# Kernel optimization log

Hardware: AMD Instinct MI355X
Metric: run time of the kernel (lower is better)

Reference implementation:

```python
import jax, jax.numpy as jnp
import numpy as np
from math import sqrt

V, D, H, HD, L, F, P, NL = 32000, 768, 12, 64, 12, 3072, 2048, 2
B, S = 8, 1024
EPS = 1e-5


def setup_inputs() -> dict:
    key = jax.random.key(0)
    ks = jax.random.split(key, 12)
    n = lambda k, sh: (jax.random.normal(k, sh, jnp.float32) * 0.02)
    return {
        'tokens': jax.random.randint(ks[0], (B, S), 0, V, dtype=jnp.int32),
        'tok_emb': n(ks[1], (V, D)),
        'pos_emb': n(ks[2], (P, D)),
        'emb_ln_s': jnp.ones((D,), jnp.float32), 'emb_ln_b': jnp.zeros((D,), jnp.float32),
        'Wq': n(ks[3], (L, H, D, HD)), 'bq': jnp.zeros((L, H, HD), jnp.float32),
        'Wk': n(ks[4], (L, H, D, HD)), 'bk': jnp.zeros((L, H, HD), jnp.float32),
        'Wv': n(ks[5], (L, H, D, HD)), 'bv': jnp.zeros((L, H, HD), jnp.float32),
        'Wo': n(ks[6], (L, D, D)), 'bo': jnp.zeros((L, D), jnp.float32),
        'ln1_s': jnp.ones((L, D), jnp.float32), 'ln1_b': jnp.zeros((L, D), jnp.float32),
        'ln2_s': jnp.ones((L, D), jnp.float32), 'ln2_b': jnp.zeros((L, D), jnp.float32),
        'W1': n(ks[7], (L, D, F)), 'b1': jnp.zeros((L, F), jnp.float32),
        'W2': n(ks[8], (L, F, D)), 'b2': jnp.zeros((L, D), jnp.float32),
        'Wc': n(ks[9], (D, NL)), 'bc': jnp.zeros((NL,), jnp.float32),
    }


def _ln(x, s, b):
    m = jnp.mean(x, -1, keepdims=True)
    v = jnp.mean((x - m) ** 2, -1, keepdims=True)
    return (x - m) * jax.lax.rsqrt(v + EPS) * s + b


def reference(tokens, tok_emb, pos_emb, emb_ln_s, emb_ln_b,
              Wq, bq, Wk, bk, Wv, bv, Wo, bo,
              ln1_s, ln1_b, ln2_s, ln2_b, W1, b1, W2, b2, Wc, bc):
    b, s = tokens.shape
    # embeddings (dropout is eval-mode identity)
    x = tok_emb[tokens] + pos_emb[:s][None, :, :]          # [b, s, D]
    x = _ln(x, emb_ln_s, emb_ln_b)
    scale = 1.0 / sqrt(HD)
    for l in range(L):
        xn = _ln(x, ln1_s[l], ln1_b[l])
        q = jnp.einsum('bsd,hdk->bhsk', xn, Wq[l]) + bq[l][:, None, :]
        k = jnp.einsum('bsd,hdk->bhsk', xn, Wk[l]) + bk[l][:, None, :]
        v = jnp.einsum('bsd,hdk->bhsk', xn, Wv[l]) + bv[l][:, None, :]
        scores = jnp.einsum('bhsk,bhtk->bhst', q, k) * scale   # [b,H,s,s]
        w = jax.nn.softmax(scores, axis=-1)
        o = jnp.einsum('bhst,bhtk->bhsk', w, v)                # [b,H,s,HD]
        o = o.transpose(0, 2, 1, 3).reshape(b, s, D)           # concat heads
        x = x + o @ Wo[l] + bo[l]
        xn = _ln(x, ln2_s[l], ln2_b[l])
        h = jax.nn.gelu(xn @ W1[l] + b1[l], approximate=False)
        x = x + h @ W2[l] + b2[l]
    # CLS token -> classifier (dropout identity)
    return x[:, 0, :] @ Wc + bc                                # [b, NL]
```

## Files before the change

### kernel.cpp

```cpp
#include <hip/hip_runtime.h>
#include <hip/hip_bf16.h>
#include <math.h>

#define B_   8
#define S_   1024
#define D_   768
#define H_   12
#define HD_  64
#define L_   12
#define F_   3072
#define NTOK 8192

typedef __bf16 bf16x8 __attribute__((ext_vector_type(8)));
typedef float  f32x4  __attribute__((ext_vector_type(4)));
typedef unsigned short u16;

static __device__ __forceinline__ unsigned short f2bf_bits(float f) {
    __hip_bfloat16 h = __float2bfloat16(f);
    return __builtin_bit_cast(unsigned short, h);
}
static __device__ __forceinline__ float bf2f(unsigned short u) {
    unsigned int t = ((unsigned int)u) << 16;
    return __builtin_bit_cast(float, t);
}
static __device__ __forceinline__ void gload16(const void* g, void* l) {
    __builtin_amdgcn_global_load_lds(
        (__attribute__((address_space(1))) void*)g,
        (__attribute__((address_space(3))) void*)l, 16, 0, 0);
}

__global__ __launch_bounds__(256)
void prep_ln_kernel(const float* __restrict__ Wq, const float* __restrict__ Wk,
                    const float* __restrict__ Wv, const float* __restrict__ Wo,
                    const float* __restrict__ W1, const float* __restrict__ W2,
                    int l, __hip_bfloat16* __restrict__ wbuf,
                    const float* __restrict__ xin, const float* __restrict__ gam,
                    const float* __restrict__ bet, __hip_bfloat16* __restrict__ xnout)
{
    __shared__ u16 T[64][68];
    if (blockIdx.x >= 1728) {
        const int row  = (blockIdx.x - 1728)*4 + (threadIdx.x >> 6);
        const int lane = threadIdx.x & 63;
        const float* xr = xin + (size_t)row * D_;
        float v[12]; float s1 = 0.f, s2 = 0.f;
#pragma unroll
        for (int c = 0; c < 3; ++c) {
            float4 t = *(const float4*)(xr + c*256 + lane*4);
            v[c*4+0]=t.x; v[c*4+1]=t.y; v[c*4+2]=t.z; v[c*4+3]=t.w;
            s1 += t.x+t.y+t.z+t.w;
            s2 += t.x*t.x + t.y*t.y + t.z*t.z + t.w*t.w;
        }
#pragma unroll
        for (int off = 32; off > 0; off >>= 1) { s1 += __shfl_xor(s1, off); s2 += __shfl_xor(s2, off); }
        const float mean = s1 * (1.f/768.f);
        const float rstd = rsqrtf(s2*(1.f/768.f) - mean*mean + 1e-5f);
        unsigned short* op = (unsigned short*)xnout + (size_t)row * D_;
#pragma unroll
        for (int c = 0; c < 3; ++c) {
            const int base = c*256 + lane*4;
            float4 g = *(const float4*)(gam + base);
            float4 bb = *(const float4*)(bet + base);
            ushort4 pk;
            pk.x = f2bf_bits((v[c*4+0]-mean)*rstd*g.x + bb.x);
            pk.y = f2bf_bits((v[c*4+1]-mean)*rstd*g.y + bb.y);
            pk.z = f2bf_bits((v[c*4+2]-mean)*rstd*g.z + bb.z);
            pk.w = f2bf_bits((v[c*4+3]-mean)*rstd*g.w + bb.w);
            *(ushort4*)(op + base) = pk;
        }
        return;
    }
    const int id = blockIdx.x;
    const float* src; __hip_bfloat16* dst;
    int R, C, r0, c0;
    if (id < 432) {
        int dtile = id % 12, t = id / 12;
        int which = t / 12, h = t % 12;
        src = (which == 0 ? Wq : which == 1 ? Wk : Wv) + (size_t)(l*12 + h) * 768 * 64;
        dst = wbuf + (size_t)(which*768 + h*64) * 768;
        R = 768; C = 64; r0 = dtile * 64; c0 = 0;
    } else if (id < 576) {
        int t = id - 432;
        src = Wo + (size_t)l * 768 * 768;
        dst = wbuf + 1769472;
        R = 768; C = 768; r0 = (t / 12) * 64; c0 = (t % 12) * 64;
    } else if (id < 1152) {
        int t = id - 576;
        src = W1 + (size_t)l * 768 * 3072;
        dst = wbuf + 2359296;
        R = 768; C = 3072; r0 = (t % 12) * 64; c0 = (t / 12) * 64;
    } else {
        int t = id - 1152;
        src = W2 + (size_t)l * 3072 * 768;
        dst = wbuf + 4718592;
        R = 3072; C = 768; r0 = (t / 12) * 64; c0 = (t % 12) * 64;
    }
    const int t = threadIdx.x;
    const int row = t >> 2, part = t & 3;
#pragma unroll
    for (int j = 0; j < 4; ++j) {
        const int c4 = (part + j*4) * 4;
        float4 v = *(const float4*)(src + (size_t)(r0 + row) * C + c0 + c4);
        T[c4+0][row] = f2bf_bits(v.x);
        T[c4+1][row] = f2bf_bits(v.y);
        T[c4+2][row] = f2bf_bits(v.z);
        T[c4+3][row] = f2bf_bits(v.w);
    }
    __syncthreads();
    const int c = t >> 2;
    u16* drow = (u16*)dst + (size_t)(c0 + c) * R + r0;
#pragma unroll
    for (int j = 0; j < 4; ++j) {
        const int r4 = (part + j*4) * 4;
        ushort4 pk = *(const ushort4*)&T[c][r4];
        *(ushort4*)(drow + r4) = pk;
    }
}

__global__ __launch_bounds__(256)
void prep_bqkv_kernel(const float* __restrict__ bq, const float* __restrict__ bk,
                      const float* __restrict__ bv, float* __restrict__ bqkv)
{
    int i = blockIdx.x * 256 + threadIdx.x;
    int l = i / 2304, c = i % 2304;
    int which = c / 768, hk = c % 768;
    const float* src = which == 0 ? bq : which == 1 ? bk : bv;
    bqkv[i] = src[l*768 + hk];
}

__global__ __launch_bounds__(256)
void embed_ln_kernel(const int* __restrict__ tokens, const float* __restrict__ tok_emb,
                     const float* __restrict__ pos_emb, const float* __restrict__ gam,
                     const float* __restrict__ bet, float* __restrict__ x)
{
    const int row  = blockIdx.x*4 + (threadIdx.x >> 6);
    const int lane = threadIdx.x & 63;
    const int s    = row & (S_-1);
    const int tok  = tokens[row];
    const float* te = tok_emb + (size_t)tok * D_;
    const float* pe = pos_emb + (size_t)s   * D_;
    float v[12]; float s1 = 0.f, s2 = 0.f;
#pragma unroll
    for (int c = 0; c < 3; ++c) {
        const int base = c*256 + lane*4;
        float4 a = *(const float4*)(te + base);
        float4 p = *(const float4*)(pe + base);
        float t0 = a.x+p.x, t1 = a.y+p.y, t2 = a.z+p.z, t3 = a.w+p.w;
        v[c*4+0]=t0; v[c*4+1]=t1; v[c*4+2]=t2; v[c*4+3]=t3;
        s1 += t0+t1+t2+t3;
        s2 += t0*t0 + t1*t1 + t2*t2 + t3*t3;
    }
#pragma unroll
    for (int off = 32; off > 0; off >>= 1) { s1 += __shfl_xor(s1, off); s2 += __shfl_xor(s2, off); }
    const float mean = s1 * (1.f/768.f);
    const float rstd = rsqrtf(s2*(1.f/768.f) - mean*mean + 1e-5f);
    float* xr = x + (size_t)row * D_;
#pragma unroll
    for (int c = 0; c < 3; ++c) {
        const int base = c*256 + lane*4;
        float4 g = *(const float4*)(gam + base);
        float4 bb = *(const float4*)(bet + base);
        float4 o;
        o.x = (v[c*4+0]-mean)*rstd*g.x + bb.x;
        o.y = (v[c*4+1]-mean)*rstd*g.y + bb.y;
        o.z = (v[c*4+2]-mean)*rstd*g.z + bb.z;
        o.w = (v[c*4+3]-mean)*rstd*g.w + bb.w;
        *(float4*)(xr + base) = o;
    }
}

__global__ __launch_bounds__(256)
void ln_kernel(const float* __restrict__ xin, const float* __restrict__ gam,
               const float* __restrict__ bet, __hip_bfloat16* __restrict__ out)
{
    const int row  = blockIdx.x*4 + (threadIdx.x >> 6);
    const int lane = threadIdx.x & 63;
    const float* xr = xin + (size_t)row * D_;
    float v[12]; float s1 = 0.f, s2 = 0.f;
#pragma unroll
    for (int c = 0; c < 3; ++c) {
        float4 t = *(const float4*)(xr + c*256 + lane*4);
        v[c*4+0]=t.x; v[c*4+1]=t.y; v[c*4+2]=t.z; v[c*4+3]=t.w;
        s1 += t.x+t.y+t.z+t.w;
        s2 += t.x*t.x + t.y*t.y + t.z*t.z + t.w*t.w;
    }
#pragma unroll
    for (int off = 32; off > 0; off >>= 1) { s1 += __shfl_xor(s1, off); s2 += __shfl_xor(s2, off); }
    const float mean = s1 * (1.f/768.f);
    const float rstd = rsqrtf(s2*(1.f/768.f) - mean*mean + 1e-5f);
    unsigned short* op = (unsigned short*)out + (size_t)row * D_;
#pragma unroll
    for (int c = 0; c < 3; ++c) {
        const int base = c*256 + lane*4;
        float4 g = *(const float4*)(gam + base);
        float4 bb = *(const float4*)(bet + base);
        ushort4 pk;
        pk.x = f2bf_bits((v[c*4+0]-mean)*rstd*g.x + bb.x);
        pk.y = f2bf_bits((v[c*4+1]-mean)*rstd*g.y + bb.y);
        pk.z = f2bf_bits((v[c*4+2]-mean)*rstd*g.z + bb.z);
        pk.w = f2bf_bits((v[c*4+3]-mean)*rstd*g.w + bb.w);
        *(ushort4*)(op + base) = pk;
    }
}

template<int EPI>
__global__ __launch_bounds__(512, 2)
void gemm256_kernel(const __hip_bfloat16* __restrict__ A,
                    const __hip_bfloat16* __restrict__ Bt,
                    const float* __restrict__ bias,
                    __hip_bfloat16* __restrict__ outb,
                    __hip_bfloat16* __restrict__ outv,
                    int N, int K, int nTiles)
{
    __shared__ __align__(16) char smem[49152];
    char* const As0 = smem;
    char* const As1 = smem + 16384;
    char* const Bs0 = smem + 32768;
    char* const Bs1 = smem + 40960;

    const int tid  = threadIdx.x;
    const int lane = tid & 63;
    const int wid  = tid >> 6;

    const int nwg   = gridDim.x;
    const int chunk = nwg >> 3;
    const int bid   = blockIdx.x;
    const int swz   = (bid & 7) * chunk + (bid >> 3);
    const int m0 = (swz / nTiles) * 256;
    const int n0 = (swz % nTiles) * 128;

    const int l4 = lane >> 2;
    const int sswz = ((lane & 3) ^ ((l4 >> 1) & 3)) * 8;
    const __hip_bfloat16* aSrc = A  + (size_t)(m0 + wid*16 + l4) * K + sswz;
    const __hip_bfloat16* bSrc = Bt + (size_t)(n0 + wid*16 + l4) * K + sswz;
    const int sOff = wid*1024 + lane*16;

    f32x4 acc[4][4] = {};
    const int wm = wid >> 1, wn = wid & 1;
    const int cl = lane & 15, hi = lane >> 4;

    int aoff[4], boff[4];
#pragma unroll
    for (int m = 0; m < 4; ++m) {
        const int row = wm*64 + m*16 + cl;
        aoff[m] = row*64 + ((hi ^ ((row >> 1) & 3)) << 4);
    }
#pragma unroll
    for (int n = 0; n < 4; ++n) {
        const int row = wn*64 + n*16 + cl;
        boff[n] = row*64 + ((hi ^ ((row >> 1) & 3)) << 4);
    }

    auto STAGE = [&](char* aBuf, char* bBuf, int kt) {
        gload16(aSrc + kt,                  aBuf + sOff);
        gload16(aSrc + kt + (size_t)128*K,  aBuf + 8192 + sOff);
        gload16(bSrc + kt,                  bBuf + sOff);
    };

    const int NT = K >> 5;
    STAGE(As0, Bs0, 0);
    STAGE(As1, Bs1, 32);

    for (int t = 0; t < NT; ++t) {
        if (t < NT - 1) asm volatile("s_waitcnt vmcnt(3)" ::: "memory");
        else            asm volatile("s_waitcnt vmcnt(0)" ::: "memory");
        __builtin_amdgcn_s_barrier();

        char* const ac = (t & 1) ? As1 : As0;
        char* const bc = (t & 1) ? Bs1 : Bs0;
        bf16x8 af[4], bfr[4];
#pragma unroll
        for (int m = 0; m < 4; ++m) af[m]  = *(const bf16x8*)(ac + aoff[m]);
#pragma unroll
        for (int n = 0; n < 4; ++n) bfr[n] = *(const bf16x8*)(bc + boff[n]);
        asm volatile("s_waitcnt lgkmcnt(0)" ::: "memory");
        __builtin_amdgcn_sched_barrier(0);
        __builtin_amdgcn_s_barrier();

        if (t + 2 < NT) STAGE(ac, bc, (t + 2) << 5);

        __builtin_amdgcn_s_setprio(1);
#pragma unroll
        for (int m = 0; m < 4; ++m)
#pragma unroll
            for (int n = 0; n < 4; ++n)
                acc[m][n] = __builtin_amdgcn_mfma_f32_16x16x32_bf16(af[m], bfr[n], acc[m][n], 0, 0, 0);
        __builtin_amdgcn_s_setprio(0);
    }

    const bool vpath = (EPI == 0) && (n0 >= 1536);

    if (!vpath) {
        const int strideN = (EPI == 0) ? 1536 : N;
#pragma unroll
        for (int n = 0; n < 4; ++n) {
            const int col = n0 + wn*64 + n*16 + cl;
            const float bv = bias[col];
#pragma unroll
            for (int m = 0; m < 4; ++m) {
#pragma unroll
                for (int i = 0; i < 4; ++i) {
                    const int row = m0 + wm*64 + m*16 + hi*4 + i;
                    float v = acc[m][n][i] + bv;
                    if constexpr (EPI == 1) {
                        const float y = 0.7978845608f * (v + 0.044715f*v*v*v);
                        const float e = __expf(-2.0f * fabsf(y));
                        const float th = (1.0f - e) / (1.0f + e);
                        v = 0.5f * v * (1.0f + copysignf(th, y));
                    }
                    outb[(size_t)row*strideN + col] = __float2bfloat16(v);
                }
            }
        }
    } else {
        const int hdbase = n0 - 1536;
        const int bb = m0 >> 10;
#pragma unroll
        for (int half = 0; half < 2; ++half) {
            __syncthreads();
            if ((wm >> 1) == half) {
#pragma unroll
                for (int n = 0; n < 4; ++n) {
                    const int hdl = wn*64 + n*16 + cl;
                    const float bv = bias[n0 + hdl];
#pragma unroll
                    for (int m = 0; m < 4; ++m) {
                        const int sl = (wm & 1)*64 + m*16 + hi*4;
                        ushort4 pk;
                        pk.x = f2bf_bits(acc[m][n][0] + bv);
                        pk.y = f2bf_bits(acc[m][n][1] + bv);
                        pk.z = f2bf_bits(acc[m][n][2] + bv);
                        pk.w = f2bf_bits(acc[m][n][3] + bv);
                        *(ushort4*)(smem + hdl*256 + ((((sl >> 3) ^ (hdl & 15))) << 4)
                                         + (sl & 7)*2) = pk;
                    }
                }
            }
            __syncthreads();
            const int hdl2 = tid >> 2;
            const int q4   = tid & 3;
            u16* dst = (u16*)outv + ((size_t)(bb*768) + hdbase + hdl2)*1024
                                  + (m0 & 1023) + half*128;
#pragma unroll
            for (int j = 0; j < 4; ++j) {
                const int ch = q4*4 + j;
                const int slot = ch ^ (hdl2 & 15);
                *(float4*)((char*)dst + ch*16) = *(const float4*)(smem + hdl2*256 + (slot << 4));
            }
        }
    }
}

__global__ __launch_bounds__(256)
void gemm_res_kernel(const __hip_bfloat16* __restrict__ A,
                     const __hip_bfloat16* __restrict__ Bt,
                     const float* __restrict__ bias,
                     float* __restrict__ outf,
                     int N, int K, int nTiles)
{
    __shared__ __align__(16) char smem[49152];
    char* const As0 = smem;
    char* const As1 = smem + 8192;
    char* const Bs0 = smem + 16384;
    char* const Bs1 = smem + 32768;

    const int tid  = threadIdx.x;
    const int lane = tid & 63;
    const int wid  = tid >> 6;

    const int nwg   = gridDim.x;
    const int chunk = nwg >> 3;
    const int bid   = blockIdx.x;
    const int swz   = (bid & 7) * chunk + (bid >> 3);
    const int m0 = (swz / nTiles) * 64;
    const int n0 = (swz % nTiles) * 128;

    const int lrow = lane >> 3;
    const int scol = ((lane & 7) ^ lrow) * 8;
    const __hip_bfloat16* aSrc = A  + (size_t)(m0 + wid*16 + lrow) * K + scol;
    const __hip_bfloat16* bSrc = Bt + (size_t)(n0 + wid*32 + lrow) * K + scol;
    const int aOff = wid*2048 + lane*16;
    const int bOff = wid*4096 + lane*16;

    f32x4 acc[2][4] = {};
    const int wm = wid >> 1, wn = wid & 1;
    const int cl = lane & 15, hi = lane >> 4;

    auto STAGE = [&](char* aBuf, char* bBuf, int kt) {
#pragma unroll
        for (int i = 0; i < 2; ++i)
            gload16(aSrc + kt + (size_t)i*8*K, aBuf + aOff + i*1024);
#pragma unroll
        for (int i = 0; i < 4; ++i)
            gload16(bSrc + kt + (size_t)i*8*K, bBuf + bOff + i*1024);
    };

    const int NT = K >> 6;
    STAGE(As0, Bs0, 0);
    STAGE(As1, Bs1, 64);

    for (int t = 0; t < NT; ++t) {
        if (t < NT - 1) asm volatile("s_waitcnt vmcnt(6)" ::: "memory");
        else            asm volatile("s_waitcnt vmcnt(0)" ::: "memory");
        __builtin_amdgcn_s_barrier();

        char* const ac = (t & 1) ? As1 : As0;
        char* const bc = (t & 1) ? Bs1 : Bs0;
        bf16x8 af[2][2], bfr[2][4];
#pragma unroll
        for (int kk = 0; kk < 2; ++kk) {
#pragma unroll
            for (int m = 0; m < 2; ++m) {
                const int row  = wm*32 + m*16 + cl;
                const int slot = ((kk<<2) + hi) ^ (row & 7);
                af[kk][m] = *(const bf16x8*)(ac + row*128 + slot*16);
            }
#pragma unroll
            for (int n = 0; n < 4; ++n) {
                const int row  = wn*64 + n*16 + cl;
                const int slot = ((kk<<2) + hi) ^ (row & 7);
                bfr[kk][n] = *(const bf16x8*)(bc + row*128 + slot*16);
            }
        }
        asm volatile("s_waitcnt lgkmcnt(0)" ::: "memory");
        __builtin_amdgcn_sched_barrier(0);
        __builtin_amdgcn_s_barrier();

        if (t + 2 < NT) STAGE(ac, bc, (t + 2) << 6);

        __builtin_amdgcn_s_setprio(1);
#pragma unroll
        for (int kk = 0; kk < 2; ++kk)
#pragma unroll
            for (int m = 0; m < 2; ++m)
#pragma unroll
                for (int n = 0; n < 4; ++n)
                    acc[m][n] = __builtin_amdgcn_mfma_f32_16x16x32_bf16(af[kk][m], bfr[kk][n], acc[m][n], 0, 0, 0);
        __builtin_amdgcn_s_setprio(0);
    }

    __syncthreads();

#pragma unroll
    for (int n = 0; n < 4; ++n) {
        const int col = wn*64 + n*16 + cl;
        const float bv = bias[n0 + col];
#pragma unroll
        for (int m = 0; m < 2; ++m) {
#pragma unroll
            for (int i = 0; i < 4; ++i) {
                const int row = wm*32 + m*16 + hi*4 + i;
                *(float*)(smem + row*512 + ((((col >> 2) ^ (row & 31))) << 4)
                               + ((col & 3) << 2)) = acc[m][n][i] + bv;
            }
        }
    }
    __syncthreads();
    const int r = tid >> 2;
    const int part = tid & 3;
    float* drow = outf + (size_t)(m0 + r) * N + n0;
#pragma unroll
    for (int j = 0; j < 8; ++j) {
        const int ch = part + j*4;
        f32x4 vv = *(const f32x4*)(smem + r*512 + ((ch ^ (r & 31)) << 4));
        float* dp = drow + ch*4;
        f32x4 g = *(const f32x4*)dp;
        g += vv;
        *(f32x4*)dp = g;
    }
}

__global__ __launch_bounds__(512)
void attn_kernel(const __hip_bfloat16* __restrict__ qkb, const __hip_bfloat16* __restrict__ vtb,
                 __hip_bfloat16* __restrict__ attno)
{
    __shared__ __align__(16) char Ks[2][8192];
    __shared__ __align__(16) char Vs[2][8192];
    __shared__ __align__(16) char Ps[16384];

    const u16* qk = (const u16*)qkb;
    const u16* vt = (const u16*)vtb;
    const int nwg = gridDim.x, bid = blockIdx.x, chunk = nwg >> 3;
    const int swz = (bid & 7) * chunk + (bid >> 3);
    const int bh = swz >> 3, qb = swz & 7;
    const int b = bh / H_, h = bh % H_;
    const int tid = threadIdx.x;
    const int lane = tid & 63, wid = tid >> 6;
    const int cl = lane & 15, hi = lane >> 4;
    const size_t browq = (size_t)(b*S_ + qb*128);

    bf16x8 qf[2];
    {
        const u16* qp = qk + (browq + wid*16 + cl)*1536 + h*64;
        qf[0] = *(const bf16x8*)(qp + hi*8);
        qf[1] = *(const bf16x8*)(qp + 32 + hi*8);
    }

    const int lrow = lane >> 3;
    const int scol = ((lane & 7) ^ lrow) * 8;
    const u16* kbase = qk + ((size_t)b*S_ + wid*8 + lrow)*1536 + 768 + h*64 + scol;
    const u16* vbase = vt + (((size_t)(b*H_ + h))*64 + wid*8 + lrow)*1024 + scol;
    const int ldst = wid*1024 + lane*16;

    f32x4 acc_o[4] = {};
    float m_run = -1e30f;
    float l_part[4] = {0.f, 0.f, 0.f, 0.f};
    char* pbase = Ps + wid*2048;

    {
        gload16(kbase, Ks[0] + ldst);
        gload16(vbase, Vs[0] + ldst);
    }

    for (int t = 0; t < 16; ++t) {
        __syncthreads();
        if (t < 15) {
            const int nb = (t+1) & 1;
            gload16(kbase + (size_t)(t+1)*64*1536, Ks[nb] + ldst);
            gload16(vbase + (t+1)*64,              Vs[nb] + ldst);
        }
        const char* ks = Ks[t & 1];
        const char* vs = Vs[t & 1];

        f32x4 sc[4] = {};
#pragma unroll
        for (int kk = 0; kk < 2; ++kk) {
            bf16x8 kf[4];
#pragma unroll
            for (int n = 0; n < 4; ++n) {
                const int row = n*16 + cl;
                kf[n] = *(const bf16x8*)(ks + row*128 + (((kk*4 + hi) ^ (cl & 7)) << 4));
            }
#pragma unroll
            for (int n = 0; n < 4; ++n)
                sc[n] = __builtin_amdgcn_mfma_f32_16x16x32_bf16(qf[kk], kf[n], sc[n], 0, 0, 0);
        }

#pragma unroll
        for (int n = 0; n < 4; ++n)
#pragma unroll
            for (int i = 0; i < 4; ++i)
                sc[n][i] *= 0.1803368801f;

        float gmax = sc[0][0];
#pragma unroll
        for (int n = 0; n < 4; ++n)
#pragma unroll
            for (int i = 0; i < 4; ++i)
                gmax = fmaxf(gmax, sc[n][i]);
        gmax = fmaxf(gmax, __shfl_xor(gmax, 1));
        gmax = fmaxf(gmax, __shfl_xor(gmax, 2));
        gmax = fmaxf(gmax, __shfl_xor(gmax, 4));
        gmax = fmaxf(gmax, __shfl_xor(gmax, 8));
        if (gmax > m_run + 5.7707801636f) {
            const float corr = exp2f(m_run - gmax);
            m_run = gmax;
#pragma unroll
            for (int i = 0; i < 4; ++i) l_part[i] *= corr;
#pragma unroll
            for (int nd = 0; nd < 4; ++nd)
#pragma unroll
                for (int i = 0; i < 4; ++i)
                    acc_o[nd][i] *= corr;
        }

#pragma unroll
        for (int n = 0; n < 4; ++n) {
#pragma unroll
            for (int i = 0; i < 4; ++i) {
                const float e = exp2f(sc[n][i] - m_run);
                l_part[i] += e;
                const int q = hi*4 + i;
                const int slot = (n*2 + (cl >> 3)) ^ (q & 7);
                *(u16*)(pbase + q*128 + slot*16 + (cl & 7)*2) = f2bf_bits(e);
            }
        }

        asm volatile("s_waitcnt lgkmcnt(0)" ::: "memory");
        __builtin_amdgcn_sched_barrier(0);

#pragma unroll
        for (int kk = 0; kk < 2; ++kk) {
            const bf16x8 pf = *(const bf16x8*)(pbase + cl*128 + (((kk*4 + hi) ^ (cl & 7)) << 4));
            bf16x8 vf[4];
#pragma unroll
            for (int nd = 0; nd < 4; ++nd) {
                const int d = nd*16 + cl;
                vf[nd] = *(const bf16x8*)(vs + d*128 + (((kk*4 + hi) ^ (d & 7)) << 4));
            }
#pragma unroll
            for (int nd = 0; nd < 4; ++nd)
                acc_o[nd] = __builtin_amdgcn_mfma_f32_16x16x32_bf16(pf, vf[nd], acc_o[nd], 0, 0, 0);
        }
    }

    u16* op = (u16*)attno;
#pragma unroll
    for (int i = 0; i < 4; ++i) {
        float l = l_part[i];
        l += __shfl_xor(l, 1);
        l += __shfl_xor(l, 2);
        l += __shfl_xor(l, 4);
        l += __shfl_xor(l, 8);
        const float inv = 1.f / l;
        const size_t row = browq + wid*16 + hi*4 + i;
#pragma unroll
        for (int nd = 0; nd < 4; ++nd)
            op[row*768 + h*64 + nd*16 + cl] = f2bf_bits(acc_o[nd][i] * inv);
    }
}

__global__ __launch_bounds__(256)
void cls_kernel(const float* __restrict__ x, const float* __restrict__ Wc,
                const float* __restrict__ bc, float* __restrict__ out)
{
    const int b = blockIdx.x;
    const float* xr = x + (size_t)b * S_ * D_;
    float a0 = 0.f, a1 = 0.f;
    for (int d = threadIdx.x; d < 768; d += 256) {
        float xv = xr[d];
        a0 += xv * Wc[d*2+0];
        a1 += xv * Wc[d*2+1];
    }
#pragma unroll
    for (int off = 32; off > 0; off >>= 1) { a0 += __shfl_xor(a0, off); a1 += __shfl_xor(a1, off); }
    __shared__ float r0[4], r1[4];
    const int w = threadIdx.x >> 6;
    if ((threadIdx.x & 63) == 0) { r0[w] = a0; r1[w] = a1; }
    __syncthreads();
    if (threadIdx.x == 0) {
        out[b*2+0] = r0[0]+r0[1]+r0[2]+r0[3] + bc[0];
        out[b*2+1] = r1[0]+r1[1]+r1[2]+r1[3] + bc[1];
    }
}

extern "C" void kernel_launch(void* const* d_in, const int* in_sizes, int n_in,
                              void* d_out, int out_size, void* d_ws, size_t ws_size,
                              hipStream_t stream)
{
    const int*   tokens  = (const int*)  d_in[0];
    const float* tok_emb = (const float*)d_in[1];
    const float* pos_emb = (const float*)d_in[2];
    const float* e_s     = (const float*)d_in[3];
    const float* e_b     = (const float*)d_in[4];
    const float* Wq      = (const float*)d_in[5];
    const float* bq      = (const float*)d_in[6];
    const float* Wk      = (const float*)d_in[7];
    const float* bk      = (const float*)d_in[8];
    const float* Wv      = (const float*)d_in[9];
    const float* bv      = (const float*)d_in[10];
    const float* Wo      = (const float*)d_in[11];
    const float* bo      = (const float*)d_in[12];
    const float* l1s     = (const float*)d_in[13];
    const float* l1b     = (const float*)d_in[14];
    const float* l2s     = (const float*)d_in[15];
    const float* l2b     = (const float*)d_in[16];
    const float* W1      = (const float*)d_in[17];
    const float* b1      = (const float*)d_in[18];
    const float* W2      = (const float*)d_in[19];
    const float* b2      = (const float*)d_in[20];
    const float* Wc      = (const float*)d_in[21];
    const float* bc      = (const float*)d_in[22];
    (void)in_sizes; (void)n_in; (void)out_size;

    if (ws_size < 102346752) return;

    char* ws = (char*)d_ws;
    __hip_bfloat16* wbuf = (__hip_bfloat16*)(ws + 0);
    float*          bqkv = (float*)(ws + 14155776);
    float*          x    = (float*)(ws + 14266368);
    __hip_bfloat16* xn   = (__hip_bfloat16*)(ws + 39432192);
    __hip_bfloat16* qk   = (__hip_bfloat16*)(ws + 52015104);
    __hip_bfloat16* vT   = (__hip_bfloat16*)(ws + 77180928);
    __hip_bfloat16* att  = (__hip_bfloat16*)(ws + 89763840);
    __hip_bfloat16* hbuf = qk;

    __hip_bfloat16* wqkv_t = wbuf;
    __hip_bfloat16* wo_t   = wbuf + 1769472;
    __hip_bfloat16* w1_t   = wbuf + 2359296;
    __hip_bfloat16* w2_t   = wbuf + 4718592;

    prep_bqkv_kernel<<<108, 256, 0, stream>>>(bq, bk, bv, bqkv);
    embed_ln_kernel<<<2048, 256, 0, stream>>>(tokens, tok_emb, pos_emb, e_s, e_b, x);

    for (int l = 0; l < L_; ++l) {
        prep_ln_kernel<<<3776, 256, 0, stream>>>(Wq, Wk, Wv, Wo, W1, W2, l, wbuf,
                                                 x, l1s + l*768, l1b + l*768, xn);
        gemm256_kernel<0><<<576, 512, 0, stream>>>(xn, wqkv_t, bqkv + l*2304, qk, vT, 2304, 768, 18);
        attn_kernel<<<768, 512, 0, stream>>>(qk, vT, att);
        gemm_res_kernel<<<768, 256, 0, stream>>>(att, wo_t, bo + l*768, x, 768, 768, 6);
        ln_kernel<<<2048, 256, 0, stream>>>(x, l2s + l*768, l2b + l*768, xn);
        gemm256_kernel<1><<<768, 512, 0, stream>>>(xn, w1_t, b1 + l*3072, hbuf, nullptr, 3072, 768, 24);
        gemm_res_kernel<<<768, 256, 0, stream>>>(hbuf, w2_t, b2 + l*768, x, 768, 3072, 6);
    }
    cls_kernel<<<8, 256, 0, stream>>>(x, Wc, bc, (float*)d_out);
}
```

Baseline: 2.985 ms.

## Use 128x128 tiles with K=32 stages in residual GEMM; pre-scale Q in attention

The residual-add GEMM moves from 64x128 tiles with a K-step of 64 to 128x128 tiles with a K-step of 32. This doubles the MFMA work per loaded fragment and halves the grid, and a two-pass epilogue keeps shared memory at 32KB so two blocks can share a CU. In attention, Q is multiplied by the softmax scale once at load time instead of scaling every score tile, and the P-store addresses and max tree are precomputed. Risks are fewer workgroups (384) on a large GPU, more barriers per K and one extra bf16 rounding of the scaled Q.

Result: slower. 3.063 ms (+2.6%).

```diff
diff --git a/kernel.cpp b/kernel.cpp
--- a/kernel.cpp
+++ b/kernel.cpp
@@ -350,18 +350,18 @@
     }
 }
 
-__global__ __launch_bounds__(256)
-void gemm_res_kernel(const __hip_bfloat16* __restrict__ A,
-                     const __hip_bfloat16* __restrict__ Bt,
-                     const float* __restrict__ bias,
-                     float* __restrict__ outf,
-                     int N, int K, int nTiles)
-{
-    __shared__ __align__(16) char smem[49152];
+__global__ __launch_bounds__(256, 2)
+void gemm128_res_kernel(const __hip_bfloat16* __restrict__ A,
+                        const __hip_bfloat16* __restrict__ Bt,
+                        const float* __restrict__ bias,
+                        float* __restrict__ outf,
+                        int N, int K, int nTiles)
+{
+    __shared__ __align__(16) char smem[32768];
     char* const As0 = smem;
     char* const As1 = smem + 8192;
     char* const Bs0 = smem + 16384;
-    char* const Bs1 = smem + 32768;
+    char* const Bs1 = smem + 24576;
 
     const int tid  = threadIdx.x;
     const int lane = tid & 63;
@@ -371,101 +371,102 @@
     const int chunk = nwg >> 3;
     const int bid   = blockIdx.x;
     const int swz   = (bid & 7) * chunk + (bid >> 3);
-    const int m0 = (swz / nTiles) * 64;
+    const int m0 = (swz / nTiles) * 128;
     const int n0 = (swz % nTiles) * 128;
 
-    const int lrow = lane >> 3;
-    const int scol = ((lane & 7) ^ lrow) * 8;
-    const __hip_bfloat16* aSrc = A  + (size_t)(m0 + wid*16 + lrow) * K + scol;
-    const __hip_bfloat16* bSrc = Bt + (size_t)(n0 + wid*32 + lrow) * K + scol;
-    const int aOff = wid*2048 + lane*16;
-    const int bOff = wid*4096 + lane*16;
-
-    f32x4 acc[2][4] = {};
+    const int l4 = lane >> 2;
+    const int sswz = ((lane & 3) ^ ((l4 >> 1) & 3)) * 8;
+    const __hip_bfloat16* aSrc = A  + (size_t)(m0 + wid*32 + l4) * K + sswz;
+    const __hip_bfloat16* bSrc = Bt + (size_t)(n0 + wid*32 + l4) * K + sswz;
+    const int sOff = wid*2048 + lane*16;
+
+    f32x4 acc[4][4] = {};
     const int wm = wid >> 1, wn = wid & 1;
     const int cl = lane & 15, hi = lane >> 4;
 
+    int aoff[4], boff[4];
+#pragma unroll
+    for (int m = 0; m < 4; ++m) {
+        const int row = wm*64 + m*16 + cl;
+        aoff[m] = row*64 + ((hi ^ ((row >> 1) & 3)) << 4);
+    }
+#pragma unroll
+    for (int n = 0; n < 4; ++n) {
+        const int row = wn*64 + n*16 + cl;
+        boff[n] = row*64 + ((hi ^ ((row >> 1) & 3)) << 4);
+    }
+
     auto STAGE = [&](char* aBuf, char* bBuf, int kt) {
 #pragma unroll
-        for (int i = 0; i < 2; ++i)
-            gload16(aSrc + kt + (size_t)i*8*K, aBuf + aOff + i*1024);
-#pragma unroll
-        for (int i = 0; i < 4; ++i)
-            gload16(bSrc + kt + (size_t)i*8*K, bBuf + bOff + i*1024);
+        for (int i = 0; i < 2; ++i) {
+            gload16(aSrc + kt + (size_t)i*16*K, aBuf + sOff + i*1024);
+            gload16(bSrc + kt + (size_t)i*16*K, bBuf + sOff + i*1024);
+        }
     };
 
-    const int NT = K >> 6;
+    const int NT = K >> 5;
     STAGE(As0, Bs0, 0);
-    STAGE(As1, Bs1, 64);
+    STAGE(As1, Bs1, 32);
 
     for (int t = 0; t < NT; ++t) {
-        if (t < NT - 1) asm volatile("s_waitcnt vmcnt(6)" ::: "memory");
+        if (t < NT - 1) asm volatile("s_waitcnt vmcnt(4)" ::: "memory");
         else            asm volatile("s_waitcnt vmcnt(0)" ::: "memory");
         __builtin_amdgcn_s_barrier();
 
         char* const ac = (t & 1) ? As1 : As0;
         char* const bc = (t & 1) ? Bs1 : Bs0;
-        bf16x8 af[2][2], bfr[2][4];
-#pragma unroll
-        for (int kk = 0; kk < 2; ++kk) {
-#pragma unroll
-            for (int m = 0; m < 2; ++m) {
-                const int row  = wm*32 + m*16 + cl;
-                const int slot = ((kk<<2) + hi) ^ (row & 7);
-                af[kk][m] = *(const bf16x8*)(ac + row*128 + slot*16);
-            }
-#pragma unroll
-            for (int n = 0; n < 4; ++n) {
-                const int row  = wn*64 + n*16 + cl;
-                const int slot = ((kk<<2) + hi) ^ (row & 7);
-                bfr[kk][n] = *(const bf16x8*)(bc + row*128 + slot*16);
-            }
-        }
+        bf16x8 af[4], bfr[4];
+#pragma unroll
+        for (int m = 0; m < 4; ++m) af[m]  = *(const bf16x8*)(ac + aoff[m]);
+#pragma unroll
+        for (int n = 0; n < 4; ++n) bfr[n] = *(const bf16x8*)(bc + boff[n]);
         asm volatile("s_waitcnt lgkmcnt(0)" ::: "memory");
         __builtin_amdgcn_sched_barrier(0);
         __builtin_amdgcn_s_barrier();
 
-        if (t + 2 < NT) STAGE(ac, bc, (t + 2) << 6);
+        if (t + 2 < NT) STAGE(ac, bc, (t + 2) << 5);
 
         __builtin_amdgcn_s_setprio(1);
 #pragma unroll
-        for (int kk = 0; kk < 2; ++kk)
-#pragma unroll
-            for (int m = 0; m < 2; ++m)
-#pragma unroll
-                for (int n = 0; n < 4; ++n)
-                    acc[m][n] = __builtin_amdgcn_mfma_f32_16x16x32_bf16(af[kk][m], bfr[kk][n], acc[m][n], 0, 0, 0);
+        for (int m = 0; m < 4; ++m)
+#pragma unroll
+            for (int n = 0; n < 4; ++n)
+                acc[m][n] = __builtin_amdgcn_mfma_f32_16x16x32_bf16(af[m], bfr[n], acc[m][n], 0, 0, 0);
         __builtin_amdgcn_s_setprio(0);
     }
 
-    __syncthreads();
-
-#pragma unroll
-    for (int n = 0; n < 4; ++n) {
-        const int col = wn*64 + n*16 + cl;
-        const float bv = bias[n0 + col];
-#pragma unroll
-        for (int m = 0; m < 2; ++m) {
-#pragma unroll
-            for (int i = 0; i < 4; ++i) {
-                const int row = wm*32 + m*16 + hi*4 + i;
-                *(float*)(smem + row*512 + ((((col >> 2) ^ (row & 31))) << 4)
-                               + ((col & 3) << 2)) = acc[m][n][i] + bv;
+#pragma unroll
+    for (int half = 0; half < 2; ++half) {
+        __syncthreads();
+        if (wm == half) {
+#pragma unroll
+            for (int n = 0; n < 4; ++n) {
+                const int col = wn*64 + n*16 + cl;
+                const float bv = bias[n0 + col];
+#pragma unroll
+                for (int m = 0; m < 4; ++m) {
+#pragma unroll
+                    for (int i = 0; i < 4; ++i) {
+                        const int row = m*16 + hi*4 + i;
+                        *(float*)(smem + row*512 + ((((col >> 2) ^ (row & 31))) << 4)
+                                       + ((col & 3) << 2)) = acc[m][n][i] + bv;
+                    }
+                }
             }
         }
-    }
-    __syncthreads();
-    const int r = tid >> 2;
-    const int part = tid & 3;
-    float* drow = outf + (size_t)(m0 + r) * N + n0;
-#pragma unroll
-    for (int j = 0; j < 8; ++j) {
-        const int ch = part + j*4;
-        f32x4 vv = *(const f32x4*)(smem + r*512 + ((ch ^ (r & 31)) << 4));
-        float* dp = drow + ch*4;
-        f32x4 g = *(const f32x4*)dp;
-        g += vv;
-        *(f32x4*)dp = g;
+        __syncthreads();
+        const int r = tid >> 2;
+        const int part = tid & 3;
+        float* drow = outf + (size_t)(m0 + half*64 + r) * N + n0;
+#pragma unroll
+        for (int j = 0; j < 8; ++j) {
+            const int ch = part + j*4;
+            f32x4 vv = *(const f32x4*)(smem + r*512 + ((ch ^ (r & 31)) << 4));
+            float* dp = drow + ch*4;
+            f32x4 g = *(const f32x4*)dp;
+            g += vv;
+            *(f32x4*)dp = g;
+        }
     }
 }
 
@@ -490,9 +491,16 @@
 
     bf16x8 qf[2];
     {
+        const float qs = 0.1803368801f;
         const u16* qp = qk + (browq + wid*16 + cl)*1536 + h*64;
-        qf[0] = *(const bf16x8*)(qp + hi*8);
-        qf[1] = *(const bf16x8*)(qp + 32 + hi*8);
+        u16 qt[16];
+#pragma unroll
+        for (int j = 0; j < 8; ++j) {
+            qt[j]     = f2bf_bits(bf2f(qp[hi*8 + j]) * qs);
+            qt[8 + j] = f2bf_bits(bf2f(qp[32 + hi*8 + j]) * qs);
+        }
+        qf[0] = *(const bf16x8*)&qt[0];
+        qf[1] = *(const bf16x8*)&qt[8];
     }
 
     const int lrow = lane >> 3;
@@ -501,10 +509,20 @@
     const u16* vbase = vt + (((size_t)(b*H_ + h))*64 + wid*8 + lrow)*1024 + scol;
     const int ldst = wid*1024 + lane*16;
 
+    char* pbase = Ps + wid*2048;
+    char* paddr[4][4];
+#pragma unroll
+    for (int n = 0; n < 4; ++n)
+#pragma unroll
+        for (int i = 0; i < 4; ++i) {
+            const int q = hi*4 + i;
+            const int slot = (n*2 + (cl >> 3)) ^ (q & 7);
+            paddr[n][i] = pbase + q*128 + slot*16 + (cl & 7)*2;
+        }
+
     f32x4 acc_o[4] = {};
     float m_run = -1e30f;
     float l_part[4] = {0.f, 0.f, 0.f, 0.f};
-    char* pbase = Ps + wid*2048;
 
     {
         gload16(kbase, Ks[0] + ldst);
@@ -535,18 +553,15 @@
                 sc[n] = __builtin_amdgcn_mfma_f32_16x16x32_bf16(qf[kk], kf[n], sc[n], 0, 0, 0);
         }
 
-#pragma unroll
-        for (int n = 0; n < 4; ++n)
-#pragma unroll
-            for (int i = 0; i < 4; ++i)
-                sc[n][i] *= 0.1803368801f;
-
-        float gmax = sc[0][0];
-#pragma unroll
-        for (int n = 0; n < 4; ++n)
-#pragma unroll
-            for (int i = 0; i < 4; ++i)
-                gmax = fmaxf(gmax, sc[n][i]);
+        float g01, g23, gmax;
+        {
+            float a0 = fmaxf(fmaxf(sc[0][0], sc[0][1]), fmaxf(sc[0][2], sc[0][3]));
+            float a1 = fmaxf(fmaxf(sc[1][0], sc[1][1]), fmaxf(sc[1][2], sc[1][3]));
+            float a2 = fmaxf(fmaxf(sc[2][0], sc[2][1]), fmaxf(sc[2][2], sc[2][3]));
+            float a3 = fmaxf(fmaxf(sc[3][0], sc[3][1]), fmaxf(sc[3][2], sc[3][3]));
+            g01 = fmaxf(a0, a1); g23 = fmaxf(a2, a3);
+            gmax = fmaxf(g01, g23);
+        }
         gmax = fmaxf(gmax, __shfl_xor(gmax, 1));
         gmax = fmaxf(gmax, __shfl_xor(gmax, 2));
         gmax = fmaxf(gmax, __shfl_xor(gmax, 4));
@@ -569,9 +584,7 @@
             for (int i = 0; i < 4; ++i) {
                 const float e = exp2f(sc[n][i] - m_run);
                 l_part[i] += e;
-                const int q = hi*4 + i;
-                const int slot = (n*2 + (cl >> 3)) ^ (q & 7);
-                *(u16*)(pbase + q*128 + slot*16 + (cl & 7)*2) = f2bf_bits(e);
+                *(u16*)paddr[n][i] = f2bf_bits(e);
             }
         }
 
@@ -687,10 +700,10 @@
                                                  x, l1s + l*768, l1b + l*768, xn);
         gemm256_kernel<0><<<576, 512, 0, stream>>>(xn, wqkv_t, bqkv + l*2304, qk, vT, 2304, 768, 18);
         attn_kernel<<<768, 512, 0, stream>>>(qk, vT, att);
-        gemm_res_kernel<<<768, 256, 0, stream>>>(att, wo_t, bo + l*768, x, 768, 768, 6);
+        gemm128_res_kernel<<<384, 256, 0, stream>>>(att, wo_t, bo + l*768, x, 768, 768, 6);
         ln_kernel<<<2048, 256, 0, stream>>>(x, l2s + l*768, l2b + l*768, xn);
         gemm256_kernel<1><<<768, 512, 0, stream>>>(xn, w1_t, b1 + l*3072, hbuf, nullptr, 3072, 768, 24);
-        gemm_res_kernel<<<768, 256, 0, stream>>>(hbuf, w2_t, b2 + l*768, x, 768, 3072, 6);
+        gemm128_res_kernel<<<384, 256, 0, stream>>>(hbuf, w2_t, b2 + l*768, x, 768, 3072, 6);
     }
     cls_kernel<<<8, 256, 0, stream>>>(x, Wc, bc, (float*)d_out);
 }
```
